# Kernel optimization log

Measured on AMD Instinct MI355X. Metric: run time of the kernel, lower is better.

Reference implementation:

```python
import jax, jax.numpy as jnp
import numpy as np

TOKENS, IN_F, OUT_F = 16384, 4096, 4096
Q_MAX_I8 = 127.0


def setup_inputs() -> dict:
    key = jax.random.key(0)
    k1, k2, k3, k4 = jax.random.split(key, 4)
    x = jax.random.normal(k1, (TOKENS, IN_F), dtype=jnp.float32)
    # packed int4 weights: two nibbles per byte along dim=1 -> [out, in//2]
    qweight = jax.random.randint(k2, (OUT_F, IN_F // 2), 0, 256, dtype=jnp.int32)
    # per-output-channel symmetric scale (positive)
    weight_scale = jax.random.uniform(k3, (OUT_F, 1), dtype=jnp.float32) * 0.01 + 1e-4
    bias = jax.random.normal(k4, (OUT_F,), dtype=jnp.float32)
    return {"x": x, "qweight": qweight, "weight_scale": weight_scale, "bias": bias}


def _unpack_int4(qweight):
    # high nibble -> even columns, low nibble -> odd columns (pack dim=1)
    high = (qweight >> 4) - 8            # [out, in//2], values in [-8, 7]
    low = (qweight & 15) - 8
    out_f = qweight.shape[0]
    return jnp.stack([high, low], axis=-1).reshape(out_f, -1)  # [out, in]


def reference(x, qweight, weight_scale, bias):
    # dequantize int4 weight: per-output-channel symmetric scale
    w = _unpack_int4(qweight).astype(jnp.float32) * weight_scale  # [out, in]
    # dynamic per-sample symmetric int8 activation fake-quant
    max_abs = jnp.max(jnp.abs(x), axis=-1, keepdims=True)         # [tokens, 1]
    act_scale = max_abs / Q_MAX_I8
    act_scale = jnp.where(act_scale == 0, 1.0, act_scale)
    q_x = jnp.clip(jnp.round(x / act_scale), -128.0, 127.0)
    x_dq = q_x * act_scale
    return x_dq @ w.T + bias
```

## Files before the change

### kernel.cpp

```cpp
#include <hip/hip_runtime.h>
#include <cstdint>

#define TOKENS 16384
#define IN_F   4096
#define OUT_F  4096

typedef int v4i __attribute__((ext_vector_type(4)));

__device__ __forceinline__ void async_lds16(const void* g, const void* l) {
    __builtin_amdgcn_global_load_lds(
        (const __attribute__((address_space(1))) void*)(uintptr_t)g,
        (__attribute__((address_space(3))) void*)(uint32_t)(uintptr_t)l,
        16, 0, 0);
}

__global__ __launch_bounds__(256) void act_quant_kernel(
        const float* __restrict__ x,
        signed char* __restrict__ qx,
        float* __restrict__ act_scale) {
    const int row = blockIdx.x;
    const int tid = threadIdx.x;
    const float4* xr = (const float4*)(x + (size_t)row * IN_F);

    float4 v[4];
    float m = 0.f;
#pragma unroll
    for (int i = 0; i < 4; ++i) {
        v[i] = xr[i * 256 + tid];
        m = fmaxf(m, fmaxf(fmaxf(fabsf(v[i].x), fabsf(v[i].y)),
                           fmaxf(fabsf(v[i].z), fabsf(v[i].w))));
    }
#pragma unroll
    for (int off = 32; off > 0; off >>= 1)
        m = fmaxf(m, __shfl_xor(m, off, 64));
    __shared__ float wmax[4];
    if ((tid & 63) == 0) wmax[tid >> 6] = m;
    __syncthreads();
    m = fmaxf(fmaxf(wmax[0], wmax[1]), fmaxf(wmax[2], wmax[3]));

    const float inv = (m == 0.f) ? 0.f : 127.0f / m;
    if (tid == 0) act_scale[row] = (m == 0.f) ? 1.0f : m / 127.0f;

    int* qr = (int*)(qx + (size_t)row * IN_F);
#pragma unroll
    for (int i = 0; i < 4; ++i) {
        int q0 = (int)fminf(fmaxf(rintf(v[i].x * inv), -128.f), 127.f);
        int q1 = (int)fminf(fmaxf(rintf(v[i].y * inv), -128.f), 127.f);
        int q2 = (int)fminf(fmaxf(rintf(v[i].z * inv), -128.f), 127.f);
        int q3 = (int)fminf(fmaxf(rintf(v[i].w * inv), -128.f), 127.f);
        qr[i * 256 + tid] = (q0 & 255) | ((q1 & 255) << 8) |
                            ((q2 & 255) << 16) | ((q3 & 255) << 24);
    }
}

__global__ __launch_bounds__(256) void unpack_w_kernel(
        const int* __restrict__ qw,
        signed char* __restrict__ w8) {
    const size_t idx = ((size_t)blockIdx.x * 256 + threadIdx.x) * 4;
    const int4 q = *(const int4*)(qw + idx);
    const int b0 = ((((q.x >> 4) & 15) - 8) & 255);
    const int b1 = (((q.x & 15) - 8) & 255);
    const int b2 = ((((q.y >> 4) & 15) - 8) & 255);
    const int b3 = (((q.y & 15) - 8) & 255);
    const int b4 = ((((q.z >> 4) & 15) - 8) & 255);
    const int b5 = (((q.z & 15) - 8) & 255);
    const int b6 = ((((q.w >> 4) & 15) - 8) & 255);
    const int b7 = (((q.w & 15) - 8) & 255);
    int2 d;
    d.x = b0 | (b1 << 8) | (b2 << 16) | (b3 << 24);
    d.y = b4 | (b5 << 8) | (b6 << 16) | (b7 << 24);
    *(int2*)(w8 + idx * 2) = d;
}

__global__ __launch_bounds__(256, 2) void gemm_i8_kernel(
        const signed char* __restrict__ qx,
        const signed char* __restrict__ w8,
        const float* __restrict__ act_scale,
        const float* __restrict__ wscale,
        const float* __restrict__ bias,
        float* __restrict__ out) {
    __shared__ __align__(16) signed char sA[128 * 64];
    __shared__ __align__(16) signed char sB[256 * 64];

    const int nt = blockIdx.x & 15;
    const int mt = blockIdx.x >> 4;
    const int m0 = mt * 128, n0 = nt * 256;
    const int tid  = threadIdx.x;
    const int lane = tid & 63;
    const int wave = tid >> 6;
    const int wm = (wave >> 1) * 64;
    const int wn = (wave & 1) * 128;

    const int lrow = lane & 15;
    const int lcol = (lane >> 4) * 16;
    const signed char* gA0 = qx + (size_t)(m0 + 16 * (2 * wave)     + lrow) * IN_F + lcol;
    const signed char* gA1 = qx + (size_t)(m0 + 16 * (2 * wave + 1) + lrow) * IN_F + lcol;
    const signed char* gB0 = w8 + (size_t)(n0 + 16 * (4 * wave)     + lrow) * IN_F + lcol;
    const signed char* gB1 = w8 + (size_t)(n0 + 16 * (4 * wave + 1) + lrow) * IN_F + lcol;
    const signed char* gB2 = w8 + (size_t)(n0 + 16 * (4 * wave + 2) + lrow) * IN_F + lcol;
    const signed char* gB3 = w8 + (size_t)(n0 + 16 * (4 * wave + 3) + lrow) * IN_F + lcol;
    signed char* lA0 = sA + (2 * wave) * 1024;
    signed char* lA1 = lA0 + 1024;
    signed char* lB0 = sB + (4 * wave) * 1024;
    signed char* lB1 = lB0 + 1024;
    signed char* lB2 = lB0 + 2048;
    signed char* lB3 = lB0 + 3072;

    v4i acc[4][8];
#pragma unroll
    for (int i = 0; i < 4; ++i)
#pragma unroll
        for (int j = 0; j < 8; ++j) acc[i][j] = (v4i){0, 0, 0, 0};

    const signed char* fA = sA + (wm >> 4) * 1024 + lane * 16;
    const signed char* fB = sB + (wn >> 4) * 1024 + lane * 16;

    for (int k0 = 0; k0 < IN_F; k0 += 64) {
        __syncthreads();
        async_lds16(gA0 + k0, lA0);
        async_lds16(gA1 + k0, lA1);
        async_lds16(gB0 + k0, lB0);
        async_lds16(gB1 + k0, lB1);
        async_lds16(gB2 + k0, lB2);
        async_lds16(gB3 + k0, lB3);
        __syncthreads();

        v4i af[4], bf[8];
#pragma unroll
        for (int i = 0; i < 4; ++i)
            af[i] = *(const v4i*)(fA + i * 1024);
#pragma unroll
        for (int j = 0; j < 8; ++j)
            bf[j] = *(const v4i*)(fB + j * 1024);

#pragma unroll
        for (int i = 0; i < 4; ++i)
#pragma unroll
            for (int j = 0; j < 8; ++j)
                acc[i][j] = __builtin_amdgcn_mfma_i32_16x16x64_i8(
                    af[i], bf[j], acc[i][j], 0, 0, 0);
    }

    const int col_lane = lane & 15;
    const int row_q    = (lane >> 4) * 4;
    float4 as4[4];
#pragma unroll
    for (int i = 0; i < 4; ++i)
        as4[i] = *(const float4*)(act_scale + m0 + wm + i * 16 + row_q);

#pragma unroll
    for (int j = 0; j < 8; ++j) {
        const int n = n0 + wn + j * 16 + col_lane;
        const float wsn = wscale[n];
        const float bn  = bias[n];
#pragma unroll
        for (int i = 0; i < 4; ++i) {
            const int mb = m0 + wm + i * 16 + row_q;
            float* orow = out + (size_t)mb * OUT_F + n;
            const float* asp = (const float*)&as4[i];
#pragma unroll
            for (int r = 0; r < 4; ++r)
                orow[(size_t)r * OUT_F] = (float)acc[i][j][r] * (asp[r] * wsn) + bn;
        }
    }
}

extern "C" void kernel_launch(void* const* d_in, const int* in_sizes, int n_in,
                              void* d_out, int out_size, void* d_ws, size_t ws_size,
                              hipStream_t stream) {
    const float* x    = (const float*)d_in[0];
    const int*   qw   = (const int*)d_in[1];
    const float* wsc  = (const float*)d_in[2];
    const float* bias = (const float*)d_in[3];
    float* out = (float*)d_out;

    char* ws = (char*)d_ws;
    float*       act_scale = (float*)ws;
    signed char* qx        = (signed char*)(ws + 65536);
    signed char* w8        = (signed char*)(ws + 65536 + (size_t)TOKENS * IN_F);

    act_quant_kernel<<<TOKENS, 256, 0, stream>>>(x, qx, act_scale);
    unpack_w_kernel<<<(OUT_F * (IN_F / 2) / 4) / 256, 256, 0, stream>>>(qw, w8);
    gemm_i8_kernel<<<(TOKENS / 128) * (OUT_F / 256), 256, 0, stream>>>(
        qx, w8, act_scale, wsc, bias, out);
}
```

Measured before the change: 847.5 us.

## Double-buffer LDS tiles to overlap async global loads with MFMA compute

Splits the shared A/B tiles into two buffers and prefetches the next K-slice with async global-to-LDS loads while the current slice is consumed by MFMAs. Explicit vmcnt waits and raw s_barrier replace the two __syncthreads per iteration. This is meant to hide global load latency in the int8 GEMM main loop. In exchange LDS use doubles to 48KB per block, which may limit occupancy at two blocks per CU, and the hand-written waitcnt must match the six outstanding loads per stage.

```diff
diff --git a/kernel.cpp b/kernel.cpp
--- a/kernel.cpp
+++ b/kernel.cpp
@@ -79,8 +79,8 @@
         const float* __restrict__ wscale,
         const float* __restrict__ bias,
         float* __restrict__ out) {
-    __shared__ __align__(16) signed char sA[128 * 64];
-    __shared__ __align__(16) signed char sB[256 * 64];
+    __shared__ __align__(16) signed char sA[2][128 * 64];
+    __shared__ __align__(16) signed char sB[2][256 * 64];
 
     const int nt = blockIdx.x & 15;
     const int mt = blockIdx.x >> 4;
@@ -93,18 +93,14 @@
 
     const int lrow = lane & 15;
     const int lcol = (lane >> 4) * 16;
-    const signed char* gA0 = qx + (size_t)(m0 + 16 * (2 * wave)     + lrow) * IN_F + lcol;
-    const signed char* gA1 = qx + (size_t)(m0 + 16 * (2 * wave + 1) + lrow) * IN_F + lcol;
-    const signed char* gB0 = w8 + (size_t)(n0 + 16 * (4 * wave)     + lrow) * IN_F + lcol;
-    const signed char* gB1 = w8 + (size_t)(n0 + 16 * (4 * wave + 1) + lrow) * IN_F + lcol;
-    const signed char* gB2 = w8 + (size_t)(n0 + 16 * (4 * wave + 2) + lrow) * IN_F + lcol;
-    const signed char* gB3 = w8 + (size_t)(n0 + 16 * (4 * wave + 3) + lrow) * IN_F + lcol;
-    signed char* lA0 = sA + (2 * wave) * 1024;
-    signed char* lA1 = lA0 + 1024;
-    signed char* lB0 = sB + (4 * wave) * 1024;
-    signed char* lB1 = lB0 + 1024;
-    signed char* lB2 = lB0 + 2048;
-    signed char* lB3 = lB0 + 3072;
+    const signed char* gA0 = qx + (size_t)(m0 + 16 * (2 * wave) + lrow) * IN_F + lcol;
+    const signed char* gA1 = gA0 + 16 * IN_F;
+    const signed char* gB0 = w8 + (size_t)(n0 + 16 * (4 * wave) + lrow) * IN_F + lcol;
+    const signed char* gB1 = gB0 + 16 * IN_F;
+    const signed char* gB2 = gB0 + 32 * IN_F;
+    const signed char* gB3 = gB0 + 48 * IN_F;
+    const int aoff = (2 * wave) * 1024;
+    const int boff = (4 * wave) * 1024;
 
     v4i acc[4][8];
 #pragma unroll
@@ -112,19 +108,20 @@
 #pragma unroll
         for (int j = 0; j < 8; ++j) acc[i][j] = (v4i){0, 0, 0, 0};
 
-    const signed char* fA = sA + (wm >> 4) * 1024 + lane * 16;
-    const signed char* fB = sB + (wn >> 4) * 1024 + lane * 16;
+    auto STAGE = [&](int buf, int k0) {
+        signed char* a = sA[buf] + aoff;
+        signed char* b = sB[buf] + boff;
+        async_lds16(gA0 + k0, a);
+        async_lds16(gA1 + k0, a + 1024);
+        async_lds16(gB0 + k0, b);
+        async_lds16(gB1 + k0, b + 1024);
+        async_lds16(gB2 + k0, b + 2048);
+        async_lds16(gB3 + k0, b + 3072);
+    };
 
-    for (int k0 = 0; k0 < IN_F; k0 += 64) {
-        __syncthreads();
-        async_lds16(gA0 + k0, lA0);
-        async_lds16(gA1 + k0, lA1);
-        async_lds16(gB0 + k0, lB0);
-        async_lds16(gB1 + k0, lB1);
-        async_lds16(gB2 + k0, lB2);
-        async_lds16(gB3 + k0, lB3);
-        __syncthreads();
-
+    auto COMPUTE = [&](int buf) {
+        const signed char* fA = sA[buf] + (wm >> 4) * 1024 + lane * 16;
+        const signed char* fB = sB[buf] + (wn >> 4) * 1024 + lane * 16;
         v4i af[4], bf[8];
 #pragma unroll
         for (int i = 0; i < 4; ++i)
@@ -132,14 +129,30 @@
 #pragma unroll
         for (int j = 0; j < 8; ++j)
             bf[j] = *(const v4i*)(fB + j * 1024);
-
 #pragma unroll
         for (int i = 0; i < 4; ++i)
 #pragma unroll
             for (int j = 0; j < 8; ++j)
                 acc[i][j] = __builtin_amdgcn_mfma_i32_16x16x64_i8(
                     af[i], bf[j], acc[i][j], 0, 0, 0);
+    };
+
+    STAGE(0, 0);
+    int cur = 0;
+    for (int k0 = 0; k0 < IN_F - 64; k0 += 64) {
+        STAGE(cur ^ 1, k0 + 64);
+        asm volatile("s_waitcnt vmcnt(6)" ::: "memory");
+        __builtin_amdgcn_s_barrier();
+        __builtin_amdgcn_sched_barrier(0);
+        COMPUTE(cur);
+        __builtin_amdgcn_sched_barrier(0);
+        __builtin_amdgcn_s_barrier();
+        cur ^= 1;
     }
+    asm volatile("s_waitcnt vmcnt(0)" ::: "memory");
+    __builtin_amdgcn_s_barrier();
+    __builtin_amdgcn_sched_barrier(0);
+    COMPUTE(cur);
 
     const int col_lane = lane & 15;
     const int row_q    = (lane >> 4) * 4;
```

Measured after the change: 831.5 us. About the same (-1.9%).
